# Kernel optimization log

Hardware: AMD Instinct MI355X
Metric: run time of the kernel (lower is better)

Reference implementation:

```python
import jax, jax.numpy as jnp
import numpy as np

G = 64          # graphs in batch
P = 31          # original nodes per graph
N_ORIG = G * P  # 1984 original nodes
N = N_ORIG + G  # 2048 total nodes (one virtual node per graph, appended at end)
D = 512         # hidden_dim
H = 8           # num_heads
DK = D // H     # per-head dim
FF = 2048       # dim_ff
L = 4           # num_layers
NF = 32         # num_node_features
MAX_SP = 100
MAX_DEG = 100


def setup_inputs() -> dict:
    key = jax.random.key(0)
    ks = jax.random.split(key, 24)
    s = 0.02
    return {
        "x": jax.random.normal(ks[0], (N_ORIG, NF), jnp.float32),
        "sp_matrix": jax.random.randint(ks[1], (N_ORIG, N_ORIG), 0, MAX_SP + 1, jnp.int32),
        "batch_ids": jnp.concatenate([
            jnp.repeat(jnp.arange(G, dtype=jnp.int32), P),
            jnp.arange(G, dtype=jnp.int32),
        ]),
        "degrees": jax.random.randint(ks[2], (N,), 0, MAX_DEG + 1, jnp.int32),
        "init_W": jax.random.normal(ks[3], (NF, D), jnp.float32) * s,
        "init_b": jnp.zeros((D,), jnp.float32),
        "cent_emb": jax.random.normal(ks[4], (MAX_DEG + 1, D), jnp.float32) * s,
        "dist_biases": jax.random.normal(ks[5], (MAX_SP + 2,), jnp.float32) * s,
        "virt_bias": jnp.zeros((), jnp.float32),
        "Wq": jax.random.normal(ks[6], (L, H, D, DK), jnp.float32) * s,
        "bq": jnp.zeros((L, H, DK), jnp.float32),
        "Wk": jax.random.normal(ks[7], (L, H, D, DK), jnp.float32) * s,
        "bk": jnp.zeros((L, H, DK), jnp.float32),
        "Wv": jax.random.normal(ks[8], (L, H, D, DK), jnp.float32) * s,
        "bv": jnp.zeros((L, H, DK), jnp.float32),
        "Wo": jax.random.normal(ks[9], (L, D, D), jnp.float32) * s,
        "bo": jnp.zeros((L, D), jnp.float32),
        "W1": jax.random.normal(ks[10], (L, D, FF), jnp.float32) * s,
        "b1": jnp.zeros((L, FF), jnp.float32),
        "W2": jax.random.normal(ks[11], (L, FF, D), jnp.float32) * s,
        "b2": jnp.zeros((L, D), jnp.float32),
    }


def _ln(h):
    # F.layer_norm with no affine params, eps=1e-5
    m = jnp.mean(h, axis=-1, keepdims=True)
    v = jnp.var(h, axis=-1, keepdims=True)
    return (h - m) / jnp.sqrt(v + 1e-5)


def reference(x, sp_matrix, batch_ids, degrees,
              init_W, init_b, cent_emb, dist_biases, virt_bias,
              Wq, bq, Wk, bk, Wv, bv, Wo, bo, W1, b1, W2, b2):
    same = batch_ids[:, None] == batch_ids[None, :]          # attention mask [N, N]
    is_virt = jnp.arange(N) >= N_ORIG

    # B matrix: fill with last distance bias (detached: torch uses .item()),
    # overwrite orig-orig block with sp-distance biases, virtual edges with
    # virt_bias, diagonal with dist_biases[0].
    fill = jax.lax.stop_gradient(dist_biases[-1])
    B = jnp.full((N, N), fill, dtype=jnp.float32)
    sp = jnp.minimum(sp_matrix, MAX_SP)
    B = B.at[:N_ORIG, :N_ORIG].set(dist_biases[sp])
    ve = (is_virt[:, None] ^ is_virt[None, :]) & same        # virt<->non-virt, same graph
    B = jnp.where(ve, virt_bias, B)
    diag = jnp.arange(N)
    B = B.at[diag, diag].set(dist_biases[0])

    # init projection, append virtual node states, add centrality encoding
    h = x @ init_W + init_b                                  # [N_ORIG, D]
    h = jnp.concatenate([h, jnp.zeros((G, D), h.dtype)], axis=0)   # [N, D]
    h = h + cent_emb[jnp.minimum(degrees, MAX_DEG)]

    scale = 1.0 / jnp.sqrt(jnp.float32(DK))
    for l in range(L):
        hn = _ln(h)
        Q = jnp.einsum('nd,hdk->hnk', hn, Wq[l]) + bq[l][:, None, :]   # [H, N, DK]
        K = jnp.einsum('nd,hdk->hnk', hn, Wk[l]) + bk[l][:, None, :]
        V = jnp.einsum('nd,hdk->hnk', hn, Wv[l]) + bv[l][:, None, :]
        logits = jnp.einsum('hik,hjk->hij', Q, K) * scale + B          # [H, N, N]
        logits = jnp.where(same, logits, -jnp.inf)
        w = jax.nn.softmax(logits, axis=-1)
        o = jnp.einsum('hij,hjk->hik', w, V)                           # [H, N, DK]
        o = jnp.transpose(o, (1, 0, 2)).reshape(N, D)                  # concat heads
        h = o @ Wo[l] + bo[l] + h                                      # residual
        hn2 = _ln(h)
        h = h + jax.nn.relu(hn2 @ W1[l] + b1[l]) @ W2[l] + b2[l]       # FFN residual

    return h[N_ORIG:]   # virtual node states, [G, D]
```

## Files before the change

### kernel.cpp

```cpp
#include <hip/hip_runtime.h>


#define NG   64
#define NP   31
#define NORI 1984
#define NT   2048
#define DIM  512
#define NHD  8
#define DKH  64
#define FFD  2048
#define NLAY 4
#define NFEA 32

typedef __attribute__((ext_vector_type(8))) short short8;
typedef __attribute__((ext_vector_type(4))) float floatx4;

__device__ __forceinline__ unsigned short f2bf(float f) {
    union { float f; unsigned u; } v; v.f = f;
    unsigned r = v.u + 0x7fffu + ((v.u >> 16) & 1u);
    return (unsigned short)(r >> 16);
}
__device__ __forceinline__ float bf2f(unsigned short u) {
    union { unsigned u; float f; } v; v.u = ((unsigned)u) << 16;
    return v.f;
}

__global__ __launch_bounds__(256) void prep_all(
    const float* __restrict__ x, const int* __restrict__ degrees,
    const float* __restrict__ init_W, const float* __restrict__ init_b,
    const float* __restrict__ cent_emb, float* __restrict__ h,
    const int* __restrict__ sp, const float* __restrict__ db,
    const float* __restrict__ virt_bias, float* __restrict__ Bg,
    const float* __restrict__ Wq, const float* __restrict__ Wk,
    const float* __restrict__ Wv, const float* __restrict__ bq,
    const float* __restrict__ bk, const float* __restrict__ bv,
    unsigned short* __restrict__ Wqkv_t, float* __restrict__ bqkv,
    const float* __restrict__ Wo, const float* __restrict__ W1,
    const float* __restrict__ W2, unsigned short* __restrict__ Wo_t,
    unsigned short* __restrict__ W1_t, unsigned short* __restrict__ W2_t)
{
    __shared__ float tl[32][33];
    int u = blockIdx.x;
    int tid = threadIdx.x;

    if (u < 2112) {
        int n = u;
        if (n >= NT) {
            int g = n - NT;
            float vb = virt_bias[0];
            for (int e = tid; e < 1024; e += 256) {
                int i = e >> 5, j = e & 31;
                float v;
                if (i == j) v = db[0];
                else if (i < NP && j < NP) {
                    int s = sp[(size_t)(g * NP + i) * NORI + g * NP + j];
                    v = db[s < 100 ? s : 100];
                } else v = vb;
                Bg[(size_t)g * 1024 + e] = v;
            }
            return;
        }
        float* xs = &tl[0][0];
        if (n < NORI && tid < NFEA) xs[tid] = x[(size_t)n * NFEA + tid];
        __syncthreads();
        int deg = degrees[n]; if (deg > 100) deg = 100;
        for (int d = tid; d < DIM; d += 256) {
            float v = cent_emb[(size_t)deg * DIM + d];
            if (n < NORI) {
                float acc = init_b[d];
                #pragma unroll
                for (int k = 0; k < NFEA; ++k) acc += xs[k] * init_W[(size_t)k * DIM + d];
                v += acc;
            }
            h[(size_t)n * DIM + d] = v;
        }
        return;
    }
    if (u < 5208) {
        int tile = u - 2112;
        if (tile >= 3072) {
            int idx = (tile - 3072) * 256 + tid;
            if (idx < NLAY * 1536) {
                int l = idx / 1536, c = idx % 1536;
                int which = c >> 9, cc = c & 511;
                const float* b = (which == 0) ? bq : (which == 1) ? bk : bv;
                bqkv[idx] = b[(size_t)l * 512 + cc];
            }
            return;
        }
        int slice = tile >> 5;
        int tloc = tile & 31;
        int dt = tloc >> 1, kt = tloc & 1;
        int l = slice / 24; int rem = slice % 24; int which = rem >> 3; int hh = rem & 7;
        const float* W = (which == 0) ? Wq : (which == 1) ? Wk : Wv;
        const float* in = W + (size_t)(l * 8 + hh) * DIM * DKH;
        int tr = tid >> 5, tc = tid & 31;
        #pragma unroll
        for (int pp = 0; pp < 4; ++pp)
            tl[tr + pp * 8][tc] = in[(size_t)(dt * 32 + tr + pp * 8) * DKH + kt * 32 + tc];
        __syncthreads();
        unsigned short* out = Wqkv_t +
            ((size_t)l * 1536 + which * 512 + hh * 64 + kt * 32) * DIM + dt * 32;
        #pragma unroll
        for (int pp = 0; pp < 4; ++pp)
            out[(size_t)(tr + pp * 8) * DIM + tc] = f2bf(tl[tc][tr + pp * 8]);
        return;
    }
    {
        int id = u - 5208;
        const float* in; unsigned short* outp; int R, C, l, rt, ct;
        if (id < 1024) {
            l = id >> 8; int t = id & 255; rt = t >> 4; ct = t & 15;
            in = Wo; outp = Wo_t; R = 512; C = 512;
        } else if (id < 5120) {
            int t2 = id - 1024; l = t2 >> 10; int t = t2 & 1023; rt = t >> 6; ct = t & 63;
            in = W1; outp = W1_t; R = 512; C = 2048;
        } else {
            int t2 = id - 5120; l = t2 >> 10; int t = t2 & 1023; rt = t >> 4; ct = t & 15;
            in = W2; outp = W2_t; R = 2048; C = 512;
        }
        const float* ip = in + (size_t)l * R * C;
        unsigned short* op = outp + (size_t)l * R * C;
        int r0 = rt * 32, c0 = ct * 32;
        int tr = tid >> 5, tc = tid & 31;
        #pragma unroll
        for (int pp = 0; pp < 4; ++pp)
            tl[tr + pp * 8][tc] = ip[(size_t)(r0 + tr + pp * 8) * C + c0 + tc];
        __syncthreads();
        #pragma unroll
        for (int pp = 0; pp < 4; ++pp)
            op[(size_t)(c0 + tr + pp * 8) * R + r0 + tc] = f2bf(tl[tc][tr + pp * 8]);
    }
}

__global__ __launch_bounds__(256) void layernorm_bf16(
    const float* __restrict__ in, unsigned short* __restrict__ out, int row0,
    float* __restrict__ fout)
{
    int n = row0 + blockIdx.x;
    int tid = threadIdx.x;
    const float* row = in + (size_t)n * DIM;
    float v0 = row[tid], v1 = row[tid + 256];
    float s = v0 + v1;
    float sq = v0 * v0 + v1 * v1;
    #pragma unroll
    for (int off = 32; off > 0; off >>= 1) {
        s  += __shfl_down(s, off);
        sq += __shfl_down(sq, off);
    }
    __shared__ float red[8];
    int wave = tid >> 6;
    if ((tid & 63) == 0) { red[wave] = s; red[4 + wave] = sq; }
    __syncthreads();
    float ts  = red[0] + red[1] + red[2] + red[3];
    float tsq = red[4] + red[5] + red[6] + red[7];
    float m   = ts * (1.0f / DIM);
    float var = tsq * (1.0f / DIM) - m * m;
    float inv = rsqrtf(var + 1e-5f);
    out[(size_t)n * DIM + tid]       = f2bf((v0 - m) * inv);
    out[(size_t)n * DIM + tid + 256] = f2bf((v1 - m) * inv);
    if (fout) {
        fout[(size_t)(n - row0) * DIM + tid]       = v0;
        fout[(size_t)(n - row0) * DIM + tid + 256] = v1;
    }
}

template<int SPLITK>
__global__ __launch_bounds__(256) void gemm64(
    const unsigned short* __restrict__ A, const unsigned short* __restrict__ Bt,
    const float* __restrict__ bias, void* __restrict__ out,
    int Nfull, int K, int moff, int flags, int P, int C, int orow)
{
    __shared__ __align__(16) unsigned short Asl[64 * 72];
    __shared__ __align__(16) unsigned short Bsl[64 * 72];
    int id = blockIdx.x;
    int by, bx, bz;
    if (P >= 8) {
        int xcd = id & 7, t = id >> 3, G = P >> 3;
        by = xcd + 8 * (t % G);
        int r2 = t / G;
        bx = r2 % C;
        bz = r2 / C;
    } else {
        by = id % P; int r2 = id / P; bx = r2 % C; bz = r2 / C;
    }
    int tid = threadIdx.x;
    int row0 = moff + by * 64, col0 = bx * 64;
    if ((flags & 4) && col0 < 512 && row0 < NORI) return;
    int kslice = K / SPLITK;
    int kbeg = bz * kslice;
    int wave = tid >> 6, lane = tid & 63;
    int quad = lane >> 4, m16 = lane & 15;
    int mw = (wave >> 1) * 32, nw = (wave & 1) * 32;
    floatx4 acc[2][2] = {};
    for (int k0 = kbeg; k0 < kbeg + kslice; k0 += 64) {
        #pragma unroll
        for (int p = 0; p < 2; ++p) {
            int idx = (p * 256 + tid) * 8;
            int r = idx >> 6, kk = idx & 63;
            *(float4*)(Asl + r * 72 + kk) =
                *(const float4*)(A + (size_t)(row0 + r) * K + k0 + kk);
            *(float4*)(Bsl + r * 72 + kk) =
                *(const float4*)(Bt + (size_t)(col0 + r) * K + k0 + kk);
        }
        __syncthreads();
        #pragma unroll
        for (int ks = 0; ks < 64; ks += 32) {
            short8 a[2], b[2];
            #pragma unroll
            for (int mi = 0; mi < 2; ++mi)
                a[mi] = *(const short8*)(Asl + (mw + mi * 16 + m16) * 72 + ks + quad * 8);
            #pragma unroll
            for (int ni = 0; ni < 2; ++ni)
                b[ni] = *(const short8*)(Bsl + (nw + ni * 16 + m16) * 72 + ks + quad * 8);
            #pragma unroll
            for (int mi = 0; mi < 2; ++mi)
                #pragma unroll
                for (int ni = 0; ni < 2; ++ni)
                    acc[mi][ni] = __builtin_amdgcn_mfma_f32_16x16x32_bf16(
                        a[mi], b[ni], acc[mi][ni], 0, 0, 0);
        }
        __syncthreads();
    }
    if (SPLITK == 1) {
        int do_relu = flags & 1, out_bf = flags & 2;
        #pragma unroll
        for (int mi = 0; mi < 2; ++mi) {
            #pragma unroll
            for (int ni = 0; ni < 2; ++ni) {
                int col = col0 + nw + ni * 16 + m16;
                float bval = bias[col];
                #pragma unroll
                for (int rr = 0; rr < 4; ++rr) {
                    int row = row0 + mw + mi * 16 + quad * 4 + rr;
                    float v = acc[mi][ni][rr] + bval;
                    if (do_relu) v = fmaxf(v, 0.0f);
                    if (out_bf) ((unsigned short*)out)[(size_t)(row - orow) * Nfull + col] = f2bf(v);
                    else        ((float*)out)[(size_t)(row - orow) * Nfull + col] = v;
                }
            }
        }
    } else {
        float* o = (float*)out;
        float bscale = (bz == 0) ? 1.0f : 0.0f;
        #pragma unroll
        for (int mi = 0; mi < 2; ++mi) {
            #pragma unroll
            for (int ni = 0; ni < 2; ++ni) {
                int col = col0 + nw + ni * 16 + m16;
                float bval = bias[col] * bscale;
                #pragma unroll
                for (int rr = 0; rr < 4; ++rr) {
                    int row = row0 + mw + mi * 16 + quad * 4 + rr;
                    atomicAdd(&o[(size_t)(row - orow) * Nfull + col],
                              acc[mi][ni][rr] + bval);
                }
            }
        }
    }
}

__device__ __forceinline__ void stage128(
    const unsigned short* __restrict__ Abase, const unsigned short* __restrict__ Bbase,
    int K, int k0, unsigned short* Asl, unsigned short* Bsl,
    int wave, int lane, int lr, int scol)
{
    #pragma unroll
    for (int p = 0; p < 4; ++p) {
        int chunk = wave * 4 + p;
        int r = chunk * 8 + lr;
        __builtin_amdgcn_global_load_lds(
            (const __attribute__((address_space(1))) unsigned int*)
                (Abase + (size_t)r * K + k0 + scol),
            (__attribute__((address_space(3))) unsigned int*)
                (Asl + chunk * 512 + lane * 8), 16, 0, 0);
        __builtin_amdgcn_global_load_lds(
            (const __attribute__((address_space(1))) unsigned int*)
                (Bbase + (size_t)r * K + k0 + scol),
            (__attribute__((address_space(3))) unsigned int*)
                (Bsl + chunk * 512 + lane * 8), 16, 0, 0);
    }
}

template<int SPLITK>
__global__ __launch_bounds__(256) void gemm128(
    const unsigned short* __restrict__ A, const unsigned short* __restrict__ Bt,
    const float* __restrict__ bias, void* __restrict__ out,
    int Nfull, int K, int flags, int P, int C)
{
    __shared__ __align__(16) unsigned short Asl[2][128 * 64];
    __shared__ __align__(16) unsigned short Bsl[2][128 * 64];
    int id = blockIdx.x;
    int xcd = id & 7, t = id >> 3, Gp = P >> 3;
    int by = xcd + 8 * (t % Gp);
    int r2 = t / Gp;
    int bx = r2 % C;
    int bz = r2 / C;
    int tid = threadIdx.x;
    int row0 = by * 128, col0 = bx * 128;
    if ((flags & 4) && col0 < 512 && row0 + 128 <= NORI) return;
    int kslice = K / SPLITK;
    int kbeg = bz * kslice;
    int nk = kslice >> 6;
    int wave = tid >> 6, lane = tid & 63;
    int quad = lane >> 4, m16 = lane & 15;
    int mw = (wave >> 1) * 64, nw = (wave & 1) * 64;
    int lr = lane >> 3;
    int scol = ((lane & 7) ^ lr) << 3;
    int rdswz = (m16 & 7) << 4;
    const unsigned short* Abase = A + (size_t)row0 * K;
    const unsigned short* Bbase = Bt + (size_t)col0 * K;
    floatx4 acc[4][4] = {};

    stage128(Abase, Bbase, K, kbeg, Asl[0], Bsl[0], wave, lane, lr, scol);
    int cur = 0;
    for (int i = 0; i < nk; ++i) {
        if (i + 1 < nk) {
            stage128(Abase, Bbase, K, kbeg + (i + 1) * 64,
                     Asl[cur ^ 1], Bsl[cur ^ 1], wave, lane, lr, scol);
            asm volatile("s_waitcnt vmcnt(8)" ::: "memory");
        } else {
            asm volatile("s_waitcnt vmcnt(0)" ::: "memory");
        }
        __builtin_amdgcn_s_barrier();
        const char* Ac = (const char*)Asl[cur];
        const char* Bc = (const char*)Bsl[cur];
        #pragma unroll
        for (int ks = 0; ks < 64; ks += 32) {
            short8 a[4], b[4];
            int cb = (ks + quad * 8) * 2;
            #pragma unroll
            for (int mi = 0; mi < 4; ++mi)
                a[mi] = *(const short8*)(Ac + (mw + mi * 16 + m16) * 128 + (cb ^ rdswz));
            #pragma unroll
            for (int ni = 0; ni < 4; ++ni)
                b[ni] = *(const short8*)(Bc + (nw + ni * 16 + m16) * 128 + (cb ^ rdswz));
            #pragma unroll
            for (int mi = 0; mi < 4; ++mi)
                #pragma unroll
                for (int ni = 0; ni < 4; ++ni)
                    acc[mi][ni] = __builtin_amdgcn_mfma_f32_16x16x32_bf16(
                        a[mi], b[ni], acc[mi][ni], 0, 0, 0);
        }
        __builtin_amdgcn_s_barrier();
        asm volatile("" ::: "memory");
        cur ^= 1;
    }
    if (SPLITK == 1) {
        int do_relu = flags & 1, out_bf = flags & 2;
        #pragma unroll
        for (int mi = 0; mi < 4; ++mi) {
            #pragma unroll
            for (int ni = 0; ni < 4; ++ni) {
                int col = col0 + nw + ni * 16 + m16;
                float bval = bias[col];
                #pragma unroll
                for (int rr = 0; rr < 4; ++rr) {
                    int row = row0 + mw + mi * 16 + quad * 4 + rr;
                    float v = acc[mi][ni][rr] + bval;
                    if (do_relu) v = fmaxf(v, 0.0f);
                    if (out_bf) ((unsigned short*)out)[(size_t)row * Nfull + col] = f2bf(v);
                    else        ((float*)out)[(size_t)row * Nfull + col] = v;
                }
            }
        }
    } else {
        float* o = (float*)out;
        float bscale = (bz == 0) ? 1.0f : 0.0f;
        #pragma unroll
        for (int mi = 0; mi < 4; ++mi) {
            #pragma unroll
            for (int ni = 0; ni < 4; ++ni) {
                int col = col0 + nw + ni * 16 + m16;
                float bval = bias[col] * bscale;
                #pragma unroll
                for (int rr = 0; rr < 4; ++rr) {
                    int row = row0 + mw + mi * 16 + quad * 4 + rr;
                    atomicAdd(&o[(size_t)row * Nfull + col], acc[mi][ni][rr] + bval);
                }
            }
        }
    }
}

__global__ __launch_bounds__(256) void attention(
    const unsigned short* __restrict__ qkv,
    const float* __restrict__ Bg,
    unsigned short* __restrict__ O)
{
    int g = blockIdx.x >> 3;
    int hh = blockIdx.x & 7;
    __shared__ float Qs[32][65], Ks[32][65], Vs[32][65];
    __shared__ float S[32][33];
    int tid = threadIdx.x;
    int i = tid >> 3;
    int c0 = (tid & 7) * 8;
    int gn = (i < NP) ? g * NP + i : NORI + g;
    const unsigned short* base = qkv + (size_t)gn * 1536 + hh * DKH;
    short8 qv = *(const short8*)(base + c0);
    short8 kv = *(const short8*)(base + 512 + c0);
    short8 vv = *(const short8*)(base + 1024 + c0);
    #pragma unroll
    for (int j = 0; j < 8; ++j) {
        Qs[i][c0 + j] = bf2f((unsigned short)qv[j]);
        Ks[i][c0 + j] = bf2f((unsigned short)kv[j]);
        Vs[i][c0 + j] = bf2f((unsigned short)vv[j]);
    }
    __syncthreads();
    const float scale = 0.125f;
    #pragma unroll
    for (int e = 0; e < 4; ++e) {
        int idx = tid + e * 256;
        int si = idx >> 5, sj = idx & 31;
        float dot = 0.0f;
        #pragma unroll
        for (int k = 0; k < DKH; ++k) dot += Qs[si][k] * Ks[sj][k];
        S[si][sj] = dot * scale + Bg[(size_t)g * 1024 + si * 32 + sj];
    }
    __syncthreads();
    if (tid < 32) {
        float mx = -1e30f;
        #pragma unroll
        for (int j = 0; j < 32; ++j) mx = fmaxf(mx, S[tid][j]);
        float sum = 0.0f;
        #pragma unroll
        for (int j = 0; j < 32; ++j) { float e = __expf(S[tid][j] - mx); S[tid][j] = e; sum += e; }
        float inv = 1.0f / sum;
        #pragma unroll
        for (int j = 0; j < 32; ++j) S[tid][j] *= inv;
    }
    __syncthreads();
    short8 ov;
    #pragma unroll
    for (int cc = 0; cc < 8; ++cc) {
        float acc = 0.0f;
        #pragma unroll
        for (int j = 0; j < 32; ++j) acc += S[i][j] * Vs[j][c0 + cc];
        ov[cc] = (short)f2bf(acc);
    }
    *(short8*)(O + (size_t)gn * DIM + hh * DKH + c0) = ov;
}

__global__ __launch_bounds__(64) void attention_last(
    const unsigned short* __restrict__ qkv, const float* __restrict__ Bg,
    unsigned short* __restrict__ O)
{
    int g = blockIdx.x >> 3, hh = blockIdx.x & 7;
    __shared__ float Ks[32][65], Vs[32][65];
    __shared__ float Qs[64], P[32];
    int tid = threadIdx.x;
    int j = tid & 31, hf = tid >> 5;
    int gn = (j < NP) ? g * NP + j : NORI + g;
    const unsigned short* kb = qkv + (size_t)gn * 1536 + hh * DKH + 512 + hf * 32;
    #pragma unroll
    for (int c = 0; c < 32; c += 8) {
        short8 k8 = *(const short8*)(kb + c);
        short8 v8 = *(const short8*)(kb + 512 + c);
        #pragma unroll
        for (int t = 0; t < 8; ++t) {
            Ks[j][hf * 32 + c + t] = bf2f((unsigned short)k8[t]);
            Vs[j][hf * 32 + c + t] = bf2f((unsigned short)v8[t]);
        }
    }
    Qs[tid] = bf2f(qkv[(size_t)(NORI + g) * 1536 + hh * DKH + tid]);
    __syncthreads();
    float s;
    if (tid < 32) {
        float dot = 0.0f;
        #pragma unroll
        for (int k = 0; k < 64; ++k) dot += Qs[k] * Ks[tid][k];
        s = dot * 0.125f + Bg[(size_t)g * 1024 + 31 * 32 + tid];
    } else s = -1e30f;
    float mx = s;
    #pragma unroll
    for (int off = 32; off > 0; off >>= 1) mx = fmaxf(mx, __shfl_xor(mx, off));
    float e = (tid < 32) ? __expf(s - mx) : 0.0f;
    float sum = e;
    #pragma unroll
    for (int off = 32; off > 0; off >>= 1) sum += __shfl_xor(sum, off);
    if (tid < 32) P[tid] = e / sum;
    __syncthreads();
    float acc = 0.0f;
    #pragma unroll
    for (int jj = 0; jj < 32; ++jj) acc += P[jj] * Vs[jj][tid];
    O[(size_t)(NORI + g) * DIM + hh * DKH + tid] = f2bf(acc);
}

extern "C" void kernel_launch(void* const* d_in, const int* in_sizes, int n_in,
                              void* d_out, int out_size, void* d_ws, size_t ws_size,
                              hipStream_t stream)
{
    const float* x        = (const float*)d_in[0];
    const int*   sp       = (const int*)d_in[1];
    const int*   degrees  = (const int*)d_in[3];
    const float* init_W   = (const float*)d_in[4];
    const float* init_b   = (const float*)d_in[5];
    const float* cent_emb = (const float*)d_in[6];
    const float* db       = (const float*)d_in[7];
    const float* vbias    = (const float*)d_in[8];
    const float* Wq       = (const float*)d_in[9];
    const float* bq       = (const float*)d_in[10];
    const float* Wk       = (const float*)d_in[11];
    const float* bk       = (const float*)d_in[12];
    const float* Wv       = (const float*)d_in[13];
    const float* bv       = (const float*)d_in[14];
    const float* Wo       = (const float*)d_in[15];
    const float* bo       = (const float*)d_in[16];
    const float* W1       = (const float*)d_in[17];
    const float* b1       = (const float*)d_in[18];
    const float* W2       = (const float*)d_in[19];
    const float* b2       = (const float*)d_in[20];

    char* ws = (char*)d_ws;
    float*          h      = (float*)ws;          ws += (size_t)NT * DIM * 4;
    unsigned short* hn     = (unsigned short*)ws; ws += (size_t)NT * DIM * 2;
    unsigned short* o      = (unsigned short*)ws; ws += (size_t)NT * DIM * 2;
    unsigned short* qkv    = (unsigned short*)ws; ws += (size_t)NT * FFD * 2;
    float*          Bg     = (float*)ws;          ws += (size_t)NG * 1024 * 4;
    unsigned short* Wqkv_t = (unsigned short*)ws; ws += (size_t)NLAY * 1536 * DIM * 2;
    unsigned short* Wo_t   = (unsigned short*)ws; ws += (size_t)NLAY * DIM * DIM * 2;
    unsigned short* W1_t   = (unsigned short*)ws; ws += (size_t)NLAY * FFD * DIM * 2;
    unsigned short* W2_t   = (unsigned short*)ws; ws += (size_t)NLAY * DIM * FFD * 2;
    float*          bqkv   = (float*)ws;          ws += (size_t)NLAY * 1536 * 4;
    unsigned short* ffnb   = qkv;

    prep_all<<<14424, 256, 0, stream>>>(
        x, degrees, init_W, init_b, cent_emb, h, sp, db, vbias, Bg,
        Wq, Wk, Wv, bq, bk, bv, Wqkv_t, bqkv, Wo, W1, W2, Wo_t, W1_t, W2_t);

    for (int l = 0; l < NLAY - 1; ++l) {
        layernorm_bf16<<<NT, 256, 0, stream>>>(h, hn, 0, nullptr);
        gemm128<1><<<16 * 12, 256, 0, stream>>>(
            hn, Wqkv_t + (size_t)l * 1536 * DIM, bqkv + (size_t)l * 1536,
            qkv, 1536, DIM, 2, 16, 12);
        attention<<<NG * NHD, 256, 0, stream>>>(qkv, Bg, o);
        gemm128<4><<<16 * 4 * 4, 256, 0, stream>>>(
            o, Wo_t + (size_t)l * DIM * DIM, bo + (size_t)l * DIM,
            h, DIM, DIM, 0, 16, 4);
        layernorm_bf16<<<NT, 256, 0, stream>>>(h, hn, 0, nullptr);
        gemm128<1><<<16 * 16, 256, 0, stream>>>(
            hn, W1_t + (size_t)l * FFD * DIM, b1 + (size_t)l * FFD,
            ffnb, FFD, DIM, 3, 16, 16);
        gemm128<4><<<16 * 4 * 4, 256, 0, stream>>>(
            ffnb, W2_t + (size_t)l * DIM * FFD, b2 + (size_t)l * DIM,
            h, DIM, FFD, 0, 16, 4);
    }

    {
        int l = NLAY - 1;
        layernorm_bf16<<<NT, 256, 0, stream>>>(h, hn, 0, nullptr);
        gemm128<1><<<16 * 12, 256, 0, stream>>>(
            hn, Wqkv_t + (size_t)l * 1536 * DIM, bqkv + (size_t)l * 1536,
            qkv, 1536, DIM, 6, 16, 12);
        attention_last<<<NG * NHD, 64, 0, stream>>>(qkv, Bg, o);
        gemm64<8><<<1 * 8 * 8, 256, 0, stream>>>(
            o, Wo_t + (size_t)l * DIM * DIM, bo + (size_t)l * DIM,
            h, DIM, DIM, NORI, 0, 1, 8, 0);
        layernorm_bf16<<<NG, 256, 0, stream>>>(h, hn, NORI, (float*)d_out);
        gemm64<1><<<1 * 32, 256, 0, stream>>>(
            hn, W1_t + (size_t)l * FFD * DIM, b1 + (size_t)l * FFD,
            ffnb, FFD, DIM, NORI, 3, 1, 32, 0);
        gemm64<8><<<1 * 8 * 8, 256, 0, stream>>>(
            ffnb, W2_t + (size_t)l * DIM * FFD, b2 + (size_t)l * DIM,
            d_out, DIM, FFD, NORI, 0, 1, 8, NORI);
    }
}
```

Measured before the change: 451.7 us.

## Fuse per-graph attention with Wo projection and residual into one kernel

Replaces the separate attention kernel and the split-K Wo GEMM with one kernel per (graph, 128-column slice). Each block computes all 8 heads of attention for its graph into LDS, then multiplies by a Wo slice with MFMA and adds bias and residual directly into h, with no atomics. This removes a launch, the global round trip of the attention output, and atomic adds. In exchange each graph's attention is recomputed 4 times (once per column slice), and heads are processed serially within a block with many syncs, leaving only 256 blocks.

```diff
diff --git a/kernel.cpp b/kernel.cpp
--- a/kernel.cpp
+++ b/kernel.cpp
@@ -383,62 +383,126 @@
     }
 }
 
-__global__ __launch_bounds__(256) void attention(
-    const unsigned short* __restrict__ qkv,
-    const float* __restrict__ Bg,
-    unsigned short* __restrict__ O)
-{
-    int g = blockIdx.x >> 3;
-    int hh = blockIdx.x & 7;
-    __shared__ float Qs[32][65], Ks[32][65], Vs[32][65];
-    __shared__ float S[32][33];
+__global__ __launch_bounds__(256) void attn_wo(
+    const unsigned short* __restrict__ qkv, const float* __restrict__ Bg,
+    const unsigned short* __restrict__ Wo_t, const float* __restrict__ bo,
+    float* __restrict__ h)
+{
+    __shared__ __align__(16) unsigned short o_lds[32][520];
+    __shared__ __align__(16) union U {
+        struct { float Qs[32][65], Ks[32][65], Vs[32][65], S[32][33]; } p1;
+        unsigned short Bsl[128 * 64];
+    } u;
+    int id = blockIdx.x;
+    int g = id >> 2, cs = id & 3;
     int tid = threadIdx.x;
     int i = tid >> 3;
-    int c0 = (tid & 7) * 8;
-    int gn = (i < NP) ? g * NP + i : NORI + g;
-    const unsigned short* base = qkv + (size_t)gn * 1536 + hh * DKH;
-    short8 qv = *(const short8*)(base + c0);
-    short8 kv = *(const short8*)(base + 512 + c0);
-    short8 vv = *(const short8*)(base + 1024 + c0);
+    int c0q = (tid & 7) * 8;
+    int gni = (i < NP) ? g * NP + i : NORI + g;
+
+    for (int hh = 0; hh < NHD; ++hh) {
+        const unsigned short* base = qkv + (size_t)gni * 1536 + hh * DKH;
+        short8 qv = *(const short8*)(base + c0q);
+        short8 kv = *(const short8*)(base + 512 + c0q);
+        short8 vv = *(const short8*)(base + 1024 + c0q);
+        #pragma unroll
+        for (int j = 0; j < 8; ++j) {
+            u.p1.Qs[i][c0q + j] = bf2f((unsigned short)qv[j]);
+            u.p1.Ks[i][c0q + j] = bf2f((unsigned short)kv[j]);
+            u.p1.Vs[i][c0q + j] = bf2f((unsigned short)vv[j]);
+        }
+        __syncthreads();
+        #pragma unroll
+        for (int e = 0; e < 4; ++e) {
+            int idx = tid + e * 256;
+            int si = idx >> 5, sj = idx & 31;
+            float dot = 0.0f;
+            #pragma unroll
+            for (int k = 0; k < DKH; ++k) dot += u.p1.Qs[si][k] * u.p1.Ks[sj][k];
+            u.p1.S[si][sj] = dot * 0.125f + Bg[(size_t)g * 1024 + si * 32 + sj];
+        }
+        __syncthreads();
+        if (tid < 32) {
+            float mx = -1e30f;
+            #pragma unroll
+            for (int j = 0; j < 32; ++j) mx = fmaxf(mx, u.p1.S[tid][j]);
+            float sum = 0.0f;
+            #pragma unroll
+            for (int j = 0; j < 32; ++j) {
+                float e = __expf(u.p1.S[tid][j] - mx);
+                u.p1.S[tid][j] = e; sum += e;
+            }
+            float inv = 1.0f / sum;
+            #pragma unroll
+            for (int j = 0; j < 32; ++j) u.p1.S[tid][j] *= inv;
+        }
+        __syncthreads();
+        #pragma unroll
+        for (int cc = 0; cc < 8; ++cc) {
+            float acc = 0.0f;
+            #pragma unroll
+            for (int j = 0; j < 32; ++j) acc += u.p1.S[i][j] * u.p1.Vs[j][c0q + cc];
+            o_lds[i][hh * DKH + c0q + cc] = f2bf(acc);
+        }
+        __syncthreads();
+    }
+
+    int wave = tid >> 6, lane = tid & 63;
+    int quad = lane >> 4, m16 = lane & 15;
+    int nw = wave * 32;
+    int lr = lane >> 3;
+    int scol = ((lane & 7) ^ lr) << 3;
+    int rdswz = (m16 & 7) << 4;
+    int c0 = cs * 128;
+    const unsigned short* Bbase = Wo_t + (size_t)c0 * 512;
+    floatx4 acc[2][2] = {};
+    for (int k0 = 0; k0 < 512; k0 += 64) {
+        #pragma unroll
+        for (int p = 0; p < 4; ++p) {
+            int chunk = wave * 4 + p;
+            int r = chunk * 8 + lr;
+            __builtin_amdgcn_global_load_lds(
+                (const __attribute__((address_space(1))) unsigned int*)
+                    (Bbase + (size_t)r * 512 + k0 + scol),
+                (__attribute__((address_space(3))) unsigned int*)
+                    (u.Bsl + chunk * 512 + lane * 8), 16, 0, 0);
+        }
+        __syncthreads();
+        #pragma unroll
+        for (int ks = 0; ks < 64; ks += 32) {
+            short8 a[2], b[2];
+            int cb = (ks + quad * 8) * 2;
+            #pragma unroll
+            for (int mi = 0; mi < 2; ++mi)
+                a[mi] = *(const short8*)(&o_lds[mi * 16 + m16][k0 + ks + quad * 8]);
+            #pragma unroll
+            for (int ni = 0; ni < 2; ++ni)
+                b[ni] = *(const short8*)((const char*)u.Bsl +
+                        (nw + ni * 16 + m16) * 128 + (cb ^ rdswz));
+            #pragma unroll
+            for (int mi = 0; mi < 2; ++mi)
+                #pragma unroll
+                for (int ni = 0; ni < 2; ++ni)
+                    acc[mi][ni] = __builtin_amdgcn_mfma_f32_16x16x32_bf16(
+                        a[mi], b[ni], acc[mi][ni], 0, 0, 0);
+        }
+        __syncthreads();
+    }
     #pragma unroll
-    for (int j = 0; j < 8; ++j) {
-        Qs[i][c0 + j] = bf2f((unsigned short)qv[j]);
-        Ks[i][c0 + j] = bf2f((unsigned short)kv[j]);
-        Vs[i][c0 + j] = bf2f((unsigned short)vv[j]);
-    }
-    __syncthreads();
-    const float scale = 0.125f;
-    #pragma unroll
-    for (int e = 0; e < 4; ++e) {
-        int idx = tid + e * 256;
-        int si = idx >> 5, sj = idx & 31;
-        float dot = 0.0f;
-        #pragma unroll
-        for (int k = 0; k < DKH; ++k) dot += Qs[si][k] * Ks[sj][k];
-        S[si][sj] = dot * scale + Bg[(size_t)g * 1024 + si * 32 + sj];
-    }
-    __syncthreads();
-    if (tid < 32) {
-        float mx = -1e30f;
-        #pragma unroll
-        for (int j = 0; j < 32; ++j) mx = fmaxf(mx, S[tid][j]);
-        float sum = 0.0f;
-        #pragma unroll
-        for (int j = 0; j < 32; ++j) { float e = __expf(S[tid][j] - mx); S[tid][j] = e; sum += e; }
-        float inv = 1.0f / sum;
-        #pragma unroll
-        for (int j = 0; j < 32; ++j) S[tid][j] *= inv;
-    }
-    __syncthreads();
-    short8 ov;
-    #pragma unroll
-    for (int cc = 0; cc < 8; ++cc) {
-        float acc = 0.0f;
-        #pragma unroll
-        for (int j = 0; j < 32; ++j) acc += S[i][j] * Vs[j][c0 + cc];
-        ov[cc] = (short)f2bf(acc);
-    }
-    *(short8*)(O + (size_t)gn * DIM + hh * DKH + c0) = ov;
+    for (int mi = 0; mi < 2; ++mi) {
+        #pragma unroll
+        for (int ni = 0; ni < 2; ++ni) {
+            int col = c0 + nw + ni * 16 + m16;
+            float bval = bo[col];
+            #pragma unroll
+            for (int rr = 0; rr < 4; ++rr) {
+                int row = mi * 16 + quad * 4 + rr;
+                int gn = (row < NP) ? g * NP + row : NORI + g;
+                float* hp = &h[(size_t)gn * DIM + col];
+                *hp = *hp + acc[mi][ni][rr] + bval;
+            }
+        }
+    }
 }
 
 __global__ __launch_bounds__(64) void attention_last(
@@ -533,10 +597,8 @@
         gemm128<1><<<16 * 12, 256, 0, stream>>>(
             hn, Wqkv_t + (size_t)l * 1536 * DIM, bqkv + (size_t)l * 1536,
             qkv, 1536, DIM, 2, 16, 12);
-        attention<<<NG * NHD, 256, 0, stream>>>(qkv, Bg, o);
-        gemm128<4><<<16 * 4 * 4, 256, 0, stream>>>(
-            o, Wo_t + (size_t)l * DIM * DIM, bo + (size_t)l * DIM,
-            h, DIM, DIM, 0, 16, 4);
+        attn_wo<<<NG * 4, 256, 0, stream>>>(
+            qkv, Bg, Wo_t + (size_t)l * DIM * DIM, bo + (size_t)l * DIM, h);
         layernorm_bf16<<<NT, 256, 0, stream>>>(h, hn, 0, nullptr);
         gemm128<1><<<16 * 16, 256, 0, stream>>>(
             hn, W1_t + (size_t)l * FFD * DIM, b1 + (size_t)l * FFD,
```

New measurement: 540.7 us. 1.2x slower.
